# Optimization experiments

Measured on AMD Instinct MI355X. Metric: run time of the kernel, lower is better.

## Reference

```python
import jax, jax.numpy as jnp
import numpy as np

B, S, H, NH = 2, 2048, 1024, 16
HD = H // NH  # head_dim = 64
ROPE_BASE = 10000.0


def _rope(x):
    # x: [B, NH, S, HD]; LLaMA-style half-split rotary embedding
    s, d = x.shape[2], x.shape[3]
    inv_freq = 1.0 / (ROPE_BASE ** (jnp.arange(0, d, 2, dtype=jnp.float32) / d))  # [d/2]
    ang = jnp.arange(s, dtype=jnp.float32)[:, None] * inv_freq[None, :]            # [S, d/2]
    cos, sin = jnp.cos(ang), jnp.sin(ang)
    x1, x2 = x[..., : d // 2], x[..., d // 2:]
    return jnp.concatenate([x1 * cos - x2 * sin, x1 * sin + x2 * cos], axis=-1)


def setup_inputs() -> dict:
    key = jax.random.key(0)
    ks = jax.random.split(key, 9)
    hidden_states = jax.random.normal(ks[0], (B, S, H), dtype=jnp.float32)
    # causal mask: True = attend
    causal = jnp.tril(jnp.ones((S, S), dtype=bool))
    attention_mask = jnp.broadcast_to(causal[None, None, :, :], (B, 1, S, S))
    std = 0.02
    wq = jax.random.normal(ks[1], (H, NH * HD), dtype=jnp.float32) * std
    wk = jax.random.normal(ks[2], (H, NH * HD), dtype=jnp.float32) * std
    wv = jax.random.normal(ks[3], (H, NH * HD), dtype=jnp.float32) * std
    wo = jax.random.normal(ks[4], (NH * HD, H), dtype=jnp.float32) * std
    bq = jnp.zeros((NH * HD,), dtype=jnp.float32)
    bk = jnp.zeros((NH * HD,), dtype=jnp.float32)
    bv = jnp.zeros((NH * HD,), dtype=jnp.float32)
    bo = jnp.zeros((H,), dtype=jnp.float32)
    return {"hidden_states": hidden_states, "attention_mask": attention_mask,
            "wq": wq, "bq": bq, "wk": wk, "bk": bk, "wv": wv, "bv": bv,
            "wo": wo, "bo": bo}


def _split_heads(x):
    b, s, _ = x.shape
    return jnp.transpose(x.reshape(b, s, NH, HD), (0, 2, 1, 3))


def reference(hidden_states, attention_mask, wq, bq, wk, bk, wv, bv, wo, bo):
    q = _split_heads(hidden_states @ wq + bq)  # [B,NH,S,HD]
    k = _split_heads(hidden_states @ wk + bk)
    v = _split_heads(hidden_states @ wv + bv)
    q = _rope(q)
    k = _rope(k)
    scores = jnp.einsum('bhqd,bhkd->bhqk', q, k) / jnp.sqrt(jnp.float32(HD))
    scores = jnp.where(attention_mask, scores, jnp.float32(-1e9))
    weights = jax.nn.softmax(scores, axis=-1)
    attn = jnp.einsum('bhqk,bhkv->bhqv', weights, v)  # [B,NH,S,HD]
    attn = jnp.transpose(attn, (0, 2, 1, 3)).reshape(hidden_states.shape[0], attn.shape[2], H)
    return attn @ wo + bo
```

## Files before the change

kernel.cpp:

```cpp
#include <hip/hip_runtime.h>
#include <math.h>

typedef short bf16x8 __attribute__((ext_vector_type(8)));
typedef float f32x4  __attribute__((ext_vector_type(4)));

__device__ __forceinline__ unsigned short f2bf(float f) {
    union { float f; unsigned u; } v; v.f = f;
    unsigned r = v.u + 0x7FFFu + ((v.u >> 16) & 1u);
    return (unsigned short)(r >> 16);
}

#define GLDS16(gp, lp) __builtin_amdgcn_global_load_lds( \
    (const __attribute__((address_space(1))) void*)(gp), \
    (__attribute__((address_space(3))) void*)(lp), 16, 0, 0)

__global__ __launch_bounds__(256)
void cvt_x(const float* __restrict__ X, unsigned short* __restrict__ Xb)
{
    const size_t t = (size_t)blockIdx.x * 256 + threadIdx.x;
    const float4 a = *(const float4*)(X + t * 8);
    const float4 b = *(const float4*)(X + t * 8 + 4);
    unsigned short u[8] = { f2bf(a.x), f2bf(a.y), f2bf(a.z), f2bf(a.w),
                            f2bf(b.x), f2bf(b.y), f2bf(b.z), f2bf(b.w) };
    *(int4*)(Xb + t * 8) = *(int4*)u;
}

__global__ __launch_bounds__(256)
void transpose_w(const float* __restrict__ w0, const float* __restrict__ w1,
                 const float* __restrict__ w2, const float* __restrict__ w3,
                 unsigned short* o0, unsigned short* o1,
                 unsigned short* o2, unsigned short* o3)
{
    const float* W; unsigned short* O;
    switch (blockIdx.z) {
        case 0: W = w0; O = o0; break;
        case 1: W = w1; O = o1; break;
        case 2: W = w2; O = o2; break;
        default: W = w3; O = o3; break;
    }
    __shared__ float T[64][65];
    const int tid = threadIdx.x;
    const int n0 = blockIdx.x * 64, k0 = blockIdx.y * 64;
    #pragma unroll
    for (int i = 0; i < 4; i++) {
        const int k = (tid >> 4) + i * 16, n4 = (tid & 15) * 4;
        const float4 v = *(const float4*)(W + (size_t)(k0 + k) * 1024 + n0 + n4);
        T[k][n4] = v.x; T[k][n4+1] = v.y; T[k][n4+2] = v.z; T[k][n4+3] = v.w;
    }
    __syncthreads();
    #pragma unroll
    for (int i = 0; i < 4; i++) {
        const int n = (tid >> 4) + i * 16, k4 = (tid & 15) * 4;
        unsigned short u[4] = { f2bf(T[k4][n]), f2bf(T[k4+1][n]),
                                f2bf(T[k4+2][n]), f2bf(T[k4+3][n]) };
        *(int2*)(O + (size_t)(n0 + n) * 1024 + k0 + k4) = *(int2*)u;
    }
}

__global__ __launch_bounds__(256)
void transpose_v(const unsigned short* __restrict__ Vb, unsigned short* __restrict__ Vtb)
{
    __shared__ unsigned short T[64][72];
    const int tid = threadIdx.x, bh = blockIdx.y, s0 = blockIdx.x * 64;
    const size_t base = (size_t)bh * 2048 * 64;
    #pragma unroll
    for (int i = 0; i < 2; i++) {
        const int s = (tid >> 3) + i * 32, d8 = (tid & 7) * 8;
        *(int4*)&T[s][d8] = *(const int4*)(Vb + base + (size_t)(s0 + s) * 64 + d8);
    }
    __syncthreads();
    #pragma unroll
    for (int i = 0; i < 2; i++) {
        const int d = (tid >> 3) + i * 32, s8 = (tid & 7) * 8;
        unsigned short u[8];
        #pragma unroll
        for (int j = 0; j < 8; j++) u[j] = T[s8 + j][d];
        *(int4*)(Vtb + base + (size_t)d * 2048 + s0 + s8) = *(int4*)u;
    }
}

__global__ __launch_bounds__(256)
void qkv_gemm(const unsigned short* __restrict__ Xb,
              const unsigned short* __restrict__ Wtq, const unsigned short* __restrict__ Wtk,
              const unsigned short* __restrict__ Wtv,
              const float* __restrict__ bq, const float* __restrict__ bk,
              const float* __restrict__ bv,
              unsigned short* __restrict__ Qb, unsigned short* __restrict__ Kb,
              unsigned short* __restrict__ Vb)
{
    const unsigned short* Wt; const float* bias; unsigned short* Out;
    const int z = blockIdx.z;
    if (z == 0)      { Wt = Wtq; bias = bq; Out = Qb; }
    else if (z == 1) { Wt = Wtk; bias = bk; Out = Kb; }
    else             { Wt = Wtv; bias = bv; Out = Vb; }

    __shared__ unsigned short As[128 * 32];
    __shared__ unsigned short Bs[128 * 32];
    const int tid = threadIdx.x, lane = tid & 63, w = tid >> 6;
    const int quad = lane >> 4, c = lane & 15;
    const int wr = w >> 1, wc = w & 1;
    const int m0 = blockIdx.x * 128, n0 = blockIdx.y * 128;

    const int srow = lane >> 2, scol = (lane & 3) * 8;

    f32x4 acc[4][4];
    #pragma unroll
    for (int i = 0; i < 4; i++)
        #pragma unroll
        for (int j = 0; j < 4; j++) acc[i][j] = (f32x4){0.f, 0.f, 0.f, 0.f};

    for (int k0 = 0; k0 < 1024; k0 += 32) {
        #pragma unroll
        for (int j = 0; j < 2; j++) {
            const int r = w * 32 + j * 16;
            GLDS16(Xb + (size_t)(m0 + r + srow) * 1024 + k0 + scol, &As[r * 32]);
            GLDS16(Wt + (size_t)(n0 + r + srow) * 1024 + k0 + scol, &Bs[r * 32]);
        }
        __syncthreads();
        bf16x8 af[4], bf[4];
        #pragma unroll
        for (int rt = 0; rt < 4; rt++)
            af[rt] = *(const bf16x8*)&As[(wr * 64 + rt * 16 + c) * 32 + quad * 8];
        #pragma unroll
        for (int nt = 0; nt < 4; nt++)
            bf[nt] = *(const bf16x8*)&Bs[(wc * 64 + nt * 16 + c) * 32 + quad * 8];
        #pragma unroll
        for (int rt = 0; rt < 4; rt++)
            #pragma unroll
            for (int nt = 0; nt < 4; nt++)
                acc[rt][nt] = __builtin_amdgcn_mfma_f32_16x16x32_bf16(af[rt], bf[nt], acc[rt][nt], 0, 0, 0);
        __syncthreads();
    }

    const int h = (n0 + wc * 64) >> 6;
    const bool rope = (z < 2);
    const float kLn = 9.210340371976184f / 32.0f;
    const float inv0 = expf(-(float)c * kLn);
    const float inv1 = expf(-(float)(c + 16) * kLn);
    float bv4[4];
    #pragma unroll
    for (int nt = 0; nt < 4; nt++) bv4[nt] = bias[n0 + wc * 64 + nt * 16 + c];

    #pragma unroll
    for (int rt = 0; rt < 4; rt++) {
        #pragma unroll
        for (int reg = 0; reg < 4; reg++) {
            const int m = m0 + wr * 64 + rt * 16 + quad * 4 + reg;
            const int b = m >> 11, s = m & 2047;
            float x0 = acc[rt][0][reg] + bv4[0];
            float x1 = acc[rt][1][reg] + bv4[1];
            float x2 = acc[rt][2][reg] + bv4[2];
            float x3 = acc[rt][3][reg] + bv4[3];
            float y0 = x0, y1 = x1, y2 = x2, y3 = x3;
            if (rope) {
                float sn0, cs0, sn1, cs1;
                sincosf((float)s * inv0, &sn0, &cs0);
                sincosf((float)s * inv1, &sn1, &cs1);
                y0 = x0 * cs0 - x2 * sn0;  y2 = x0 * sn0 + x2 * cs0;
                y1 = x1 * cs1 - x3 * sn1;  y3 = x1 * sn1 + x3 * cs1;
            }
            unsigned short* dst = Out + ((size_t)(b * 16 + h) * 2048 + s) * 64;
            dst[0 * 16 + c] = f2bf(y0);
            dst[1 * 16 + c] = f2bf(y1);
            dst[2 * 16 + c] = f2bf(y2);
            dst[3 * 16 + c] = f2bf(y3);
        }
    }
}

__global__ __launch_bounds__(256)
void out_gemm(const unsigned short* __restrict__ Ab, const unsigned short* __restrict__ Wto,
              const float* __restrict__ bo, float* __restrict__ Out)
{
    __shared__ unsigned short As[128 * 32];
    __shared__ unsigned short Bs[128 * 32];
    const int tid = threadIdx.x, lane = tid & 63, w = tid >> 6;
    const int quad = lane >> 4, c = lane & 15;
    const int wr = w >> 1, wc = w & 1;
    const int m0 = blockIdx.x * 128, n0 = blockIdx.y * 128;
    const int srow = lane >> 2, scol = (lane & 3) * 8;

    f32x4 acc[4][4];
    #pragma unroll
    for (int i = 0; i < 4; i++)
        #pragma unroll
        for (int j = 0; j < 4; j++) acc[i][j] = (f32x4){0.f, 0.f, 0.f, 0.f};

    for (int k0 = 0; k0 < 1024; k0 += 32) {
        #pragma unroll
        for (int j = 0; j < 2; j++) {
            const int r = w * 32 + j * 16;
            GLDS16(Ab  + (size_t)(m0 + r + srow) * 1024 + k0 + scol, &As[r * 32]);
            GLDS16(Wto + (size_t)(n0 + r + srow) * 1024 + k0 + scol, &Bs[r * 32]);
        }
        __syncthreads();
        bf16x8 af[4], bf[4];
        #pragma unroll
        for (int rt = 0; rt < 4; rt++)
            af[rt] = *(const bf16x8*)&As[(wr * 64 + rt * 16 + c) * 32 + quad * 8];
        #pragma unroll
        for (int nt = 0; nt < 4; nt++)
            bf[nt] = *(const bf16x8*)&Bs[(wc * 64 + nt * 16 + c) * 32 + quad * 8];
        #pragma unroll
        for (int rt = 0; rt < 4; rt++)
            #pragma unroll
            for (int nt = 0; nt < 4; nt++)
                acc[rt][nt] = __builtin_amdgcn_mfma_f32_16x16x32_bf16(af[rt], bf[nt], acc[rt][nt], 0, 0, 0);
        __syncthreads();
    }
    #pragma unroll
    for (int rt = 0; rt < 4; rt++) {
        #pragma unroll
        for (int reg = 0; reg < 4; reg++) {
            const int m = m0 + wr * 64 + rt * 16 + quad * 4 + reg;
            #pragma unroll
            for (int nt = 0; nt < 4; nt++) {
                const int n = n0 + wc * 64 + nt * 16 + c;
                Out[(size_t)m * 1024 + n] = acc[rt][nt][reg] + bo[n];
            }
        }
    }
}

__global__ __launch_bounds__(256)
void attn_part(const unsigned short* __restrict__ Qb, const unsigned short* __restrict__ Kb,
               const unsigned short* __restrict__ Vtb, unsigned short* __restrict__ Ab,
               float* __restrict__ Opart, float* __restrict__ Lpart)
{
    __shared__ unsigned short Ks[64 * 72];
    __shared__ unsigned short Vs[65 * 72];
    __shared__ unsigned short Ps[4 * 16 * 72];

    const int tid = threadIdx.x, w = tid >> 6, lane = tid & 63;
    const int quad = lane >> 4, c = lane & 15;
    const int bh = blockIdx.y;
    const int x = (blockIdx.x < 32) ? (int)blockIdx.x + 16 : (int)blockIdx.x - 32;
    int i, start, len;
    if (x < 32) { i = x + 1;  start = 0;  len = (i < 16) ? i : 16; }
    else        { i = x - 15; start = 16; len = i - 16; }
    const int q0 = (i - 1) * 64;
    const bool complete = (start == 0) && (len == i);
    const size_t base = (size_t)bh * 2048 * 64;

    if (tid < 64) Vs[64 * 72 + tid] = 0x3F80;

    const int qbase = q0 + w * 16;
    const int qrow  = qbase + c;
    const size_t qoff = base + (size_t)qrow * 64;
    const bf16x8 qf0 = *(const bf16x8*)(Qb + qoff + quad * 8);
    const bf16x8 qf1 = *(const bf16x8*)(Qb + qoff + 32 + quad * 8);

    f32x4 O[4], Osum;
    Osum = (f32x4){0.f, 0.f, 0.f, 0.f};
    #pragma unroll
    for (int nt = 0; nt < 4; nt++) O[nt] = (f32x4){0.f, 0.f, 0.f, 0.f};

    const int r0s = tid >> 3, r1s = r0s + 32, c8 = (tid & 7) * 8;

    int k0 = start * 64;
    int4 kreg0 = *(const int4*)(Kb  + base + (size_t)(k0 + r0s) * 64 + c8);
    int4 kreg1 = *(const int4*)(Kb  + base + (size_t)(k0 + r1s) * 64 + c8);
    int4 vreg0 = *(const int4*)(Vtb + base + (size_t)r0s * 2048 + k0 + c8);
    int4 vreg1 = *(const int4*)(Vtb + base + (size_t)r1s * 2048 + k0 + c8);

    unsigned short* Pw = Ps + w * 16 * 72;

    for (int t = 0; t < len; t++, k0 += 64) {
        *(int4*)&Ks[(size_t)r0s * 72 + c8] = kreg0;
        *(int4*)&Ks[(size_t)r1s * 72 + c8] = kreg1;
        *(int4*)&Vs[(size_t)r0s * 72 + c8] = vreg0;
        *(int4*)&Vs[(size_t)r1s * 72 + c8] = vreg1;
        __syncthreads();

        if (t + 1 < len) {
            const int kn = k0 + 64;
            kreg0 = *(const int4*)(Kb  + base + (size_t)(kn + r0s) * 64 + c8);
            kreg1 = *(const int4*)(Kb  + base + (size_t)(kn + r1s) * 64 + c8);
            vreg0 = *(const int4*)(Vtb + base + (size_t)r0s * 2048 + kn + c8);
            vreg1 = *(const int4*)(Vtb + base + (size_t)r1s * 2048 + kn + c8);
        }

        const bool need_mask = (k0 + 63) > qbase;

        #pragma unroll
        for (int nt = 0; nt < 4; nt++) {
            const bf16x8 kf0 = *(const bf16x8*)&Ks[(nt * 16 + c) * 72 + quad * 8];
            const bf16x8 kf1 = *(const bf16x8*)&Ks[(nt * 16 + c) * 72 + 32 + quad * 8];
            f32x4 s4 = (f32x4){0.f, 0.f, 0.f, 0.f};
            s4 = __builtin_amdgcn_mfma_f32_16x16x32_bf16(kf0, qf0, s4, 0, 0, 0);
            s4 = __builtin_amdgcn_mfma_f32_16x16x32_bf16(kf1, qf1, s4, 0, 0, 0);
            const int keyb = k0 + nt * 16 + quad * 4;
            unsigned short u[4];
            #pragma unroll
            for (int reg = 0; reg < 4; reg++) {
                float p = __expf(s4[reg] * 0.125f);
                if (need_mask && (keyb + reg > qrow)) p = 0.f;
                u[reg] = f2bf(p);
            }
            *(int2*)&Pw[c * 72 + nt * 16 + quad * 4] = *(int2*)u;
        }

        const bf16x8 pa0 = *(const bf16x8*)&Pw[c * 72 + quad * 8];
        const bf16x8 pa1 = *(const bf16x8*)&Pw[c * 72 + 32 + quad * 8];
        #pragma unroll
        for (int nt = 0; nt < 4; nt++) {
            const bf16x8 vb0 = *(const bf16x8*)&Vs[(nt * 16 + c) * 72 + quad * 8];
            const bf16x8 vb1 = *(const bf16x8*)&Vs[(nt * 16 + c) * 72 + 32 + quad * 8];
            O[nt] = __builtin_amdgcn_mfma_f32_16x16x32_bf16(pa0, vb0, O[nt], 0, 0, 0);
            O[nt] = __builtin_amdgcn_mfma_f32_16x16x32_bf16(pa1, vb1, O[nt], 0, 0, 0);
        }
        const bf16x8 on0 = *(const bf16x8*)&Vs[64 * 72 + quad * 8];
        const bf16x8 on1 = *(const bf16x8*)&Vs[64 * 72 + 32 + quad * 8];
        Osum = __builtin_amdgcn_mfma_f32_16x16x32_bf16(pa0, on0, Osum, 0, 0, 0);
        Osum = __builtin_amdgcn_mfma_f32_16x16x32_bf16(pa1, on1, Osum, 0, 0, 0);
        __syncthreads();
    }

    if (complete) {
        const int b = bh >> 4, h = bh & 15;
        #pragma unroll
        for (int reg = 0; reg < 4; reg++) {
            const float inv = 1.0f / Osum[reg];
            const int q = qbase + quad * 4 + reg;
            const size_t rowoff = ((size_t)(b * 2048 + q)) * 1024 + h * 64;
            #pragma unroll
            for (int nt = 0; nt < 4; nt++)
                Ab[rowoff + nt * 16 + c] = f2bf(O[nt][reg] * inv);
        }
    } else {
        const int pslot = (i - 17) * 2 + (start ? 1 : 0);
        float* Op = Opart + ((size_t)bh * 32 + pslot) * 4096;
        float* Lp = Lpart + ((size_t)bh * 32 + pslot) * 64;
        #pragma unroll
        for (int reg = 0; reg < 4; reg++) {
            const int row = w * 16 + quad * 4 + reg;
            #pragma unroll
            for (int nt = 0; nt < 4; nt++)
                Op[(size_t)row * 64 + nt * 16 + c] = O[nt][reg];
            if (c == 0) Lp[row] = Osum[reg];
        }
    }
}

__global__ __launch_bounds__(256)
void attn_combine(const float* __restrict__ Opart, const float* __restrict__ Lpart,
                  unsigned short* __restrict__ Ab)
{
    const int tid = threadIdx.x;
    const int j = blockIdx.x, bh = blockIdx.y;
    const int q0 = (j + 16) * 64;
    const size_t s0 = ((size_t)bh * 32 + j * 2) * 4096;
    const size_t l0 = ((size_t)bh * 32 + j * 2) * 64;

    __shared__ float linv[64];
    if (tid < 64) linv[tid] = 1.0f / (Lpart[l0 + tid] + Lpart[l0 + 64 + tid]);
    __syncthreads();

    const int row = tid >> 2, col0 = (tid & 3) * 16;
    const float inv = linv[row];
    const int b = bh >> 4, h = bh & 15;
    const int q = q0 + row;
    unsigned short* dst = Ab + ((size_t)(b * 2048 + q)) * 1024 + h * 64 + col0;
    #pragma unroll
    for (int c4 = 0; c4 < 16; c4 += 4) {
        const float4 a  = *(const float4*)(Opart + s0 + (size_t)row * 64 + col0 + c4);
        const float4 bb = *(const float4*)(Opart + s0 + 4096 + (size_t)row * 64 + col0 + c4);
        dst[c4 + 0] = f2bf((a.x + bb.x) * inv);
        dst[c4 + 1] = f2bf((a.y + bb.y) * inv);
        dst[c4 + 2] = f2bf((a.z + bb.z) * inv);
        dst[c4 + 3] = f2bf((a.w + bb.w) * inv);
    }
}

extern "C" void kernel_launch(void* const* d_in, const int* in_sizes, int n_in,
                              void* d_out, int out_size, void* d_ws, size_t ws_size,
                              hipStream_t stream)
{
    const float* X  = (const float*)d_in[0];
    const float* wq = (const float*)d_in[2];
    const float* bq = (const float*)d_in[3];
    const float* wk = (const float*)d_in[4];
    const float* bk = (const float*)d_in[5];
    const float* wv = (const float*)d_in[6];
    const float* bv = (const float*)d_in[7];
    const float* wo = (const float*)d_in[8];
    const float* bo = (const float*)d_in[9];

    unsigned short* ws = (unsigned short*)d_ws;
    const size_t M1 = 1024 * 1024;
    unsigned short* Xb  = ws;
    unsigned short* Wtq = Xb  + 4 * M1;
    unsigned short* Wtk = Wtq + M1;
    unsigned short* Wtv = Wtk + M1;
    unsigned short* Wto = Wtv + M1;
    unsigned short* Qb  = Wto + M1;
    unsigned short* Kb  = Qb  + 4 * M1;
    unsigned short* Vb  = Kb  + 4 * M1;
    unsigned short* Vtb = Vb  + 4 * M1;
    unsigned short* Ab  = Vtb + 4 * M1;
    float* Opart = (float*)(Ab + 4 * M1);
    float* Lpart = Opart + (size_t)32 * 32 * 4096;

    cvt_x       <<<2048, 256, 0, stream>>>(X, Xb);
    transpose_w <<<dim3(16, 16, 4), 256, 0, stream>>>(wq, wk, wv, wo, Wtq, Wtk, Wtv, Wto);
    qkv_gemm    <<<dim3(32, 8, 3), 256, 0, stream>>>(Xb, Wtq, Wtk, Wtv, bq, bk, bv, Qb, Kb, Vb);
    transpose_v <<<dim3(32, 32), 256, 0, stream>>>(Vb, Vtb);
    attn_part   <<<dim3(48, 32), 256, 0, stream>>>(Qb, Kb, Vtb, Ab, Opart, Lpart);
    attn_combine<<<dim3(16, 32), 256, 0, stream>>>(Opart, Lpart, Ab);
    out_gemm    <<<dim3(32, 8), 256, 0, stream>>>(Ab, Wto, bo, (float*)d_out);
}
```

Measured before the change: 231.8 us.

## Fuse prep kernels, use hardware sin/cos, and vectorize head-dim stores via permutation

Merges the X conversion and weight transposes into one launch to save a kernel launch. Replaces sincosf with range-reduced hardware sin/cos intrinsics in the QKV epilogue, which lowers accuracy for large arguments. Permutes the head-dim layout so each lane writes 4 contiguous bf16 values (int2/float4 stores) in the QKV, attention and partial-output epilogues. The Wo rows are permuted to compensate, which needs the permutation to stay consistent across kernels.

```diff
diff --git a/kernel.cpp b/kernel.cpp
--- a/kernel.cpp
+++ b/kernel.cpp
@@ -14,25 +14,27 @@
     (const __attribute__((address_space(1))) void*)(gp), \
     (__attribute__((address_space(3))) void*)(lp), 16, 0, 0)
 
-__global__ __launch_bounds__(256)
-void cvt_x(const float* __restrict__ X, unsigned short* __restrict__ Xb)
-{
-    const size_t t = (size_t)blockIdx.x * 256 + threadIdx.x;
-    const float4 a = *(const float4*)(X + t * 8);
-    const float4 b = *(const float4*)(X + t * 8 + 4);
-    unsigned short u[8] = { f2bf(a.x), f2bf(a.y), f2bf(a.z), f2bf(a.w),
-                            f2bf(b.x), f2bf(b.y), f2bf(b.z), f2bf(b.w) };
-    *(int4*)(Xb + t * 8) = *(int4*)u;
-}
-
-__global__ __launch_bounds__(256)
-void transpose_w(const float* __restrict__ w0, const float* __restrict__ w1,
-                 const float* __restrict__ w2, const float* __restrict__ w3,
-                 unsigned short* o0, unsigned short* o1,
-                 unsigned short* o2, unsigned short* o3)
-{
+
+__global__ __launch_bounds__(256)
+void prep(const float* __restrict__ X, unsigned short* __restrict__ Xb,
+          const float* __restrict__ w0, const float* __restrict__ w1,
+          const float* __restrict__ w2, const float* __restrict__ w3,
+          unsigned short* o0, unsigned short* o1,
+          unsigned short* o2, unsigned short* o3)
+{
+    const int z = blockIdx.z;
+    if (z >= 4) {
+        const int lb = (z - 4) * 256 + blockIdx.y * 16 + blockIdx.x;
+        const size_t t = (size_t)lb * 256 + threadIdx.x;
+        const float4 a = *(const float4*)(X + t * 8);
+        const float4 b = *(const float4*)(X + t * 8 + 4);
+        unsigned short u[8] = { f2bf(a.x), f2bf(a.y), f2bf(a.z), f2bf(a.w),
+                                f2bf(b.x), f2bf(b.y), f2bf(b.z), f2bf(b.w) };
+        *(int4*)(Xb + t * 8) = *(int4*)u;
+        return;
+    }
     const float* W; unsigned short* O;
-    switch (blockIdx.z) {
+    switch (z) {
         case 0: W = w0; O = o0; break;
         case 1: W = w1; O = o1; break;
         case 2: W = w2; O = o2; break;
@@ -48,12 +50,28 @@
         T[k][n4] = v.x; T[k][n4+1] = v.y; T[k][n4+2] = v.z; T[k][n4+3] = v.w;
     }
     __syncthreads();
-    #pragma unroll
-    for (int i = 0; i < 4; i++) {
-        const int n = (tid >> 4) + i * 16, k4 = (tid & 15) * 4;
-        unsigned short u[4] = { f2bf(T[k4][n]), f2bf(T[k4+1][n]),
-                                f2bf(T[k4+2][n]), f2bf(T[k4+3][n]) };
-        *(int2*)(O + (size_t)(n0 + n) * 1024 + k0 + k4) = *(int2*)u;
+    if (z == 3) {
+        #pragma unroll
+        for (int i = 0; i < 4; i++) {
+            const int n = (tid >> 4) + i * 16, k4 = (tid & 15) * 4;
+            unsigned short u[4];
+            #pragma unroll
+            for (int j = 0; j < 4; j++) {
+                const int q = k4 + j;
+                const int p = (q & 3) * 16 + (q >> 2);
+                const int d = (p & 3) * 16 + (p >> 2);
+                u[j] = f2bf(T[d][n]);
+            }
+            *(int2*)(O + (size_t)(n0 + n) * 1024 + k0 + k4) = *(int2*)u;
+        }
+    } else {
+        #pragma unroll
+        for (int i = 0; i < 4; i++) {
+            const int n = (tid >> 4) + i * 16, k4 = (tid & 15) * 4;
+            unsigned short u[4] = { f2bf(T[k4][n]), f2bf(T[k4+1][n]),
+                                    f2bf(T[k4+2][n]), f2bf(T[k4+3][n]) };
+            *(int2*)(O + (size_t)(n0 + n) * 1024 + k0 + k4) = *(int2*)u;
+        }
     }
 }
 
@@ -100,7 +118,6 @@
     const int quad = lane >> 4, c = lane & 15;
     const int wr = w >> 1, wc = w & 1;
     const int m0 = blockIdx.x * 128, n0 = blockIdx.y * 128;
-
     const int srow = lane >> 2, scol = (lane & 3) * 8;
 
     f32x4 acc[4][4];
@@ -135,8 +152,9 @@
     const int h = (n0 + wc * 64) >> 6;
     const bool rope = (z < 2);
     const float kLn = 9.210340371976184f / 32.0f;
-    const float inv0 = expf(-(float)c * kLn);
-    const float inv1 = expf(-(float)(c + 16) * kLn);
+    const float TWO_PI_INV = 0.15915494309189535f;
+    const float rv0 = expf(-(float)c * kLn) * TWO_PI_INV;
+    const float rv1 = expf(-(float)(c + 16) * kLn) * TWO_PI_INV;
     float bv4[4];
     #pragma unroll
     for (int nt = 0; nt < 4; nt++) bv4[nt] = bias[n0 + wc * 64 + nt * 16 + c];
@@ -153,17 +171,18 @@
             float x3 = acc[rt][3][reg] + bv4[3];
             float y0 = x0, y1 = x1, y2 = x2, y3 = x3;
             if (rope) {
-                float sn0, cs0, sn1, cs1;
-                sincosf((float)s * inv0, &sn0, &cs0);
-                sincosf((float)s * inv1, &sn1, &cs1);
+                float r0 = (float)s * rv0;  r0 -= floorf(r0);
+                float r1 = (float)s * rv1;  r1 -= floorf(r1);
+                const float sn0 = __builtin_amdgcn_sinf(r0);
+                const float cs0 = __builtin_amdgcn_cosf(r0);
+                const float sn1 = __builtin_amdgcn_sinf(r1);
+                const float cs1 = __builtin_amdgcn_cosf(r1);
                 y0 = x0 * cs0 - x2 * sn0;  y2 = x0 * sn0 + x2 * cs0;
                 y1 = x1 * cs1 - x3 * sn1;  y3 = x1 * sn1 + x3 * cs1;
             }
+            unsigned short u[4] = { f2bf(y0), f2bf(y1), f2bf(y2), f2bf(y3) };
             unsigned short* dst = Out + ((size_t)(b * 16 + h) * 2048 + s) * 64;
-            dst[0 * 16 + c] = f2bf(y0);
-            dst[1 * 16 + c] = f2bf(y1);
-            dst[2 * 16 + c] = f2bf(y2);
-            dst[3 * 16 + c] = f2bf(y3);
+            *(int2*)(dst + c * 4) = *(int2*)u;
         }
     }
 }
@@ -322,10 +341,11 @@
         for (int reg = 0; reg < 4; reg++) {
             const float inv = 1.0f / Osum[reg];
             const int q = qbase + quad * 4 + reg;
-            const size_t rowoff = ((size_t)(b * 2048 + q)) * 1024 + h * 64;
-            #pragma unroll
-            for (int nt = 0; nt < 4; nt++)
-                Ab[rowoff + nt * 16 + c] = f2bf(O[nt][reg] * inv);
+            unsigned short u[4];
+            #pragma unroll
+            for (int nt = 0; nt < 4; nt++) u[nt] = f2bf(O[nt][reg] * inv);
+            unsigned short* dst = Ab + ((size_t)(b * 2048 + q)) * 1024 + h * 64;
+            *(int2*)(dst + c * 4) = *(int2*)u;
         }
     } else {
         const int pslot = (i - 17) * 2 + (start ? 1 : 0);
@@ -334,9 +354,8 @@
         #pragma unroll
         for (int reg = 0; reg < 4; reg++) {
             const int row = w * 16 + quad * 4 + reg;
-            #pragma unroll
-            for (int nt = 0; nt < 4; nt++)
-                Op[(size_t)row * 64 + nt * 16 + c] = O[nt][reg];
+            float4 o4 = make_float4(O[0][reg], O[1][reg], O[2][reg], O[3][reg]);
+            *(float4*)(Op + (size_t)row * 64 + c * 4) = o4;
             if (c == 0) Lp[row] = Osum[reg];
         }
     }
@@ -401,8 +420,8 @@
     float* Opart = (float*)(Ab + 4 * M1);
     float* Lpart = Opart + (size_t)32 * 32 * 4096;
 
-    cvt_x       <<<2048, 256, 0, stream>>>(X, Xb);
-    transpose_w <<<dim3(16, 16, 4), 256, 0, stream>>>(wq, wk, wv, wo, Wtq, Wtk, Wtv, Wto);
+    prep        <<<dim3(16, 16, 12), 256, 0, stream>>>(X, Xb, wq, wk, wv, wo,
+                                                       Wtq, Wtk, Wtv, Wto);
     qkv_gemm    <<<dim3(32, 8, 3), 256, 0, stream>>>(Xb, Wtq, Wtk, Wtv, bq, bk, bv, Qb, Kb, Vb);
     transpose_v <<<dim3(32, 32), 256, 0, stream>>>(Vb, Vtb);
     attn_part   <<<dim3(48, 32), 256, 0, stream>>>(Qb, Kb, Vtb, Ab, Opart, Lpart);
```

Result: no change. 228.5 us (-1.4%).
